# Kernel tuning notes

Hardware: AMD Instinct MI355X
Metric: run time of the kernel (lower is better)

## Reference

```python
import jax, jax.numpy as jnp
import numpy as np

N, S, D = 512, 64, 128   # num_nodes, seq_len, model_size
H, K = 4, 32             # num_heads, key_size
E = 4096                 # num_edges
WF = 4                   # widening_factor
EPS = 1e-5


def _alibi(num_heads, seq_len):
    slopes = 2.0 ** (-8.0 * (jnp.arange(1, num_heads + 1, dtype=jnp.float32) / num_heads))
    pos = jnp.arange(seq_len, dtype=jnp.float32)
    rel = pos[None, :] - pos[:, None]  # T - t, <= 0 in causal region
    return (slopes[:, None, None] * rel)[None]  # [1,H,S,S]


def layer_norm(x, scale, offset):
    mu = jnp.mean(x, axis=-1, keepdims=True)
    var = jnp.var(x, axis=-1, keepdims=True)
    return (x - mu) * jax.lax.rsqrt(var + EPS) * scale + offset


def segment_softmax(logits, seg, num_segments):
    maxs = jax.ops.segment_max(logits, seg, num_segments=num_segments)
    e = jnp.exp(logits - maxs[seg])
    denom = jax.ops.segment_sum(e, seg, num_segments=num_segments)
    return e / denom[seg]


def setup_inputs() -> dict:
    key = jax.random.key(0)
    ks = jax.random.split(key, 24)
    sd = 0.02
    inp = {
        'nodes': jax.random.normal(ks[0], (N, S, D), jnp.float32),
        'senders': jax.random.randint(ks[1], (E,), 0, N, jnp.int32),
        'receivers': jax.random.randint(ks[2], (E,), 0, N, jnp.int32),
        'alibi_mask': _alibi(H, S),
        'ln1_s': jnp.ones((D,)), 'ln1_b': jnp.zeros((D,)),
        'wq': jax.random.normal(ks[3], (D, H * K)) * sd, 'bq': jnp.zeros((H * K,)),
        'wk': jax.random.normal(ks[4], (D, H * K)) * sd, 'bk': jnp.zeros((H * K,)),
        'wv': jax.random.normal(ks[5], (D, H * K)) * sd, 'bv': jnp.zeros((H * K,)),
        'wo': jax.random.normal(ks[6], (H * K, D)) * sd, 'bo': jnp.zeros((D,)),
        'ln2_s': jnp.ones((D,)), 'ln2_b': jnp.zeros((D,)),
        'w1': jax.random.normal(ks[7], (D, WF * D)) * sd, 'b1': jnp.zeros((WF * D,)),
        'w2': jax.random.normal(ks[8], (WF * D, D)) * sd, 'b2': jnp.zeros((D,)),
        'ln3_s': jnp.ones((D,)), 'ln3_b': jnp.zeros((D,)),
        'w_sa': jax.random.normal(ks[9], (2 * D, D)) * sd, 'b_sa': jnp.zeros((D,)),
        'w_sq': jax.random.normal(ks[10], (D, H * D)) * sd, 'b_sq': jnp.zeros((H * D,)),
    }
    return inp


def reference(nodes, senders, receivers, alibi_mask,
              ln1_s, ln1_b, wq, bq, wk, bk, wv, bv, wo, bo,
              ln2_s, ln2_b, w1, b1, w2, b2, ln3_s, ln3_b,
              w_sa, b_sa, w_sq, b_sq):
    n, s, d = nodes.shape
    # --- node self-attention with ALiBi + causal mask ---
    xn = layer_norm(nodes, ln1_s, ln1_b)
    q = (xn @ wq + bq).reshape(n, s, H, K)
    k = (xn @ wk + bk).reshape(n, s, H, K)
    v = (xn @ wv + bv).reshape(n, s, H, K)
    logits = jnp.einsum('nthk,nThk->nhtT', q, k)
    logits = alibi_mask + logits / jnp.sqrt(jnp.float32(K))
    causal = jnp.tril(jnp.ones((1, 1, s, s), dtype=bool))
    logits = jnp.where(causal, logits, -1e30)
    w = jax.nn.softmax(logits, axis=-1)
    attn = jnp.einsum('nhtT,nThk->nthk', w, v).reshape(n, s, H * K)
    nodes = nodes + (attn @ wo + bo)  # dropout rate 0 (eval)
    # --- FFN block ---
    xn = layer_norm(nodes, ln2_s, ln2_b)
    dense = jax.nn.gelu(xn @ w1 + b1) @ w2 + b2
    nodes = layer_norm(nodes + dense, ln3_s, ln3_b)
    # --- graph message passing: gather / segment-softmax / segment-sum ---
    sent = nodes[senders]        # [E,S,D]
    recv = nodes[receivers]      # [E,S,D]
    sl = jnp.concatenate([sent, recv], axis=-1) @ w_sa + b_sa  # [E,S,D]
    aw = segment_softmax(sl, receivers, n)                     # [E,S,D]
    sq = (aw @ w_sq + b_sq).reshape(E, s, H, d)                # [E,S,H,D]
    messages = jnp.mean(sq * sent[:, :, None, :], axis=2)      # [E,S,D]
    out = jax.ops.segment_sum(messages, receivers, num_segments=n)
    return out
```

## Files before the change

kernel.cpp:

```cpp
#include <hip/hip_runtime.h>
#include <hip/hip_bf16.h>

typedef __hip_bfloat16 bf16;
typedef __attribute__((ext_vector_type(8))) __bf16 bf8v;
typedef __attribute__((ext_vector_type(4))) float  f4v;

#define NN 512
#define SSEQ 64
#define DDIM 128
#define HH 4
#define NROWS (NN*SSEQ)
#define EMAX 4096
#define ECH 64

__device__ __forceinline__ float b2f(bf16 x){ return __bfloat162float(x); }
__device__ __forceinline__ bf16 f2b(float x){ return __float2bfloat16(x); }
__device__ __forceinline__ float ldf(float x){ return x; }
__device__ __forceinline__ float ldf(bf16 x){ return b2f(x); }
__device__ __forceinline__ void stf(float* p, float v){ *p = v; }
__device__ __forceinline__ void stf(bf16* p, float v){ *p = f2b(v); }

__device__ __forceinline__ f4v mfma16(bf8v a, bf8v b, f4v c){
  return __builtin_amdgcn_mfma_f32_16x16x32_bf16(a, b, c, 0, 0, 0);
}
__device__ __forceinline__ bf8v ldfrag(const void* p){
  return __builtin_bit_cast(bf8v, *(const int4*)p);
}
__device__ __forceinline__ float gelu_f(float v){
  return 0.5f*v*(1.0f + tanhf(0.7978845608028654f*(v + 0.044715f*v*v*v)));
}

__global__ __launch_bounds__(512) void prep_all_k(
    const float* wq, const float* wk, const float* wv, const float* wo,
    const float* w1, const float* w2, const float* wsa,
    const float* w_sq, const float* b_sq,
    const float* bq, const float* bk, const float* bv,
    const int* __restrict__ receivers,
    bf16* wqkvT, bf16* woT, bf16* w1T, bf16* w2T, bf16* wsaTt,
    bf16* wbarT, float* bbar, float* qkv_bias,
    int* off, int* perm, int* chunk_cnt, int E){
  int b = blockIdx.x, t = threadIdx.x;
  if (b < 832){
    if (t >= 256) return;
    const float* W; bf16* Wt; int K, lN, rel, roff = 0;
    if      (b < 64) { W=wq;  Wt=wqkvT; K=128; lN=7; rel=b;     roff=0;   }
    else if (b <128) { W=wk;  Wt=wqkvT; K=128; lN=7; rel=b-64;  roff=128; }
    else if (b <192) { W=wv;  Wt=wqkvT; K=128; lN=7; rel=b-128; roff=256; }
    else if (b <256) { W=wo;  Wt=woT;   K=128; lN=7; rel=b-192; }
    else if (b <512) { W=w1;  Wt=w1T;   K=128; lN=9; rel=b-256; }
    else if (b <768) { W=w2;  Wt=w2T;   K=512; lN=7; rel=b-512; }
    else             { W=wsa; Wt=wsaTt; K=128; lN=7; rel=b-768; }
    int i = rel*256 + t;
    int k = i >> lN, n = i & ((1<<lN)-1);
    Wt[(size_t)(n+roff)*K + k] = f2b(W[i]);
  } else if (b < 896){
    if (t >= 256) return;
    int i = (b-832)*256 + t;
    int c = i>>7, d = i&127;
    float s = 0.f;
    #pragma unroll
    for (int h=0;h<HH;++h) s += w_sq[(size_t)c*(HH*DDIM) + h*DDIM + d];
    wbarT[d*DDIM + c] = f2b(0.25f*s);
  } else if (b < 898){
    if (t >= 256) return;
    int idx = (b-896)*256 + t;
    if (idx < 128){
      float s = 0.f;
      #pragma unroll
      for (int h=0;h<HH;++h) s += b_sq[h*DDIM + idx];
      bbar[idx] = 0.25f*s;
    } else if (idx < 512){
      int j = idx - 128;
      float v = (j<128) ? bq[j] : (j<256) ? bk[j-128] : bv[j-256];
      qkv_bias[j] = v;
    }
  } else if (b == 898){
    __shared__ int s_cnt[NN];
    s_cnt[t] = 0;
    __syncthreads();
    for (int e=t; e<E; e+=512) atomicAdd(&s_cnt[receivers[e]], 1);
    __syncthreads();
    int deg = s_cnt[t];
    int acc = 0, myrank = 0;
    for (int i=0;i<NN;++i){
      int di = s_cnt[i];
      acc    += (i<t) ? di : 0;
      myrank += ((di > deg) || (di == deg && i < t)) ? 1 : 0;
    }
    off[t] = acc;
    if (t==NN-1) off[NN] = acc + deg;
    perm[myrank] = t;
  } else {
    __shared__ int hc[NN];
    int c = b - 899;
    for (int i=t;i<NN;i+=512) hc[i]=0;
    __syncthreads();
    if (t < ECH){
      int e = c*ECH + t;
      if (e < E) atomicAdd(&hc[receivers[e]], 1);
    }
    __syncthreads();
    for (int i=t;i<NN;i+=512) chunk_cnt[(size_t)c*NN + i] = hc[i];
  }
}

__global__ __launch_bounds__(64) void slot_k(const int* __restrict__ senders,
    const int* __restrict__ receivers, const int* __restrict__ off,
    const int* __restrict__ chunk_cnt, int* __restrict__ slot_snd, int E){
  int t = threadIdx.x, c = blockIdx.x;
  int e = c*ECH + t;
  bool valid = (e < E);
  int r  = valid ? receivers[e] : -1;
  int sd = valid ? senders[e]   : 0;
  int base = 0;
  if (valid){
    base = off[r];
    for (int cp=0; cp<c; ++cp) base += chunk_cnt[(size_t)cp*NN + r];
  }
  int rank = 0;
  #pragma unroll
  for (int i=0;i<64;++i){
    int ri = __shfl(r, i);
    rank += (i < t && ri == r) ? 1 : 0;
  }
  if (valid) slot_snd[base + rank] = sd;
}

__global__ __launch_bounds__(256) void gemm_ln1qkv_k(const float* __restrict__ X,
    const float* __restrict__ lns, const float* __restrict__ lnb,
    const bf16* __restrict__ Wt, const float* __restrict__ bias,
    bf16* __restrict__ C){
  __shared__ bf16 sA[64][136];
  __shared__ bf16 sB[64][72];
  int t = threadIdx.x, bm = blockIdx.x;
  int w = t>>6, lane = t&63, ls = lane&15, lg = lane>>4;
  int wr = w>>1, wc = w&1;
  {
    int r = t>>2, q = t&3;
    float vals[32];
    const float* xr = X + (size_t)(bm*64 + r)*DDIM + q*32;
    #pragma unroll
    for (int p=0;p<8;++p){
      float4 v = *(const float4*)(xr + p*4);
      vals[p*4+0]=v.x; vals[p*4+1]=v.y; vals[p*4+2]=v.z; vals[p*4+3]=v.w;
    }
    float s=0.f, sq=0.f;
    #pragma unroll
    for (int j=0;j<32;++j){ s += vals[j]; sq += vals[j]*vals[j]; }
    s  += __shfl_xor(s, 1);  s  += __shfl_xor(s, 2);
    sq += __shfl_xor(sq, 1); sq += __shfl_xor(sq, 2);
    float mu   = s*(1.0f/DDIM);
    float var  = sq*(1.0f/DDIM) - mu*mu;
    float rstd = rsqrtf(var + 1e-5f);
    #pragma unroll
    for (int p=0;p<4;++p){
      bf16 pv[8];
      #pragma unroll
      for (int j=0;j<8;++j){
        int cidx = q*32 + p*8 + j;
        pv[j] = f2b((vals[p*8+j]-mu)*rstd*lns[cidx] + lnb[cidx]);
      }
      *(int4*)(&sA[r][q*32 + p*8]) = *(const int4*)pv;
    }
  }
  for (int bn=0; bn<6; ++bn){
    f4v acc[2][2] = {};
    for (int ks=0; ks<128; ks+=64){
      __syncthreads();
      #pragma unroll
      for (int p=0;p<2;++p){
        int r = p*32 + (t>>3), cc = (t&7)*8;
        *(int4*)(&sB[r][cc]) = *(const int4*)(Wt + (size_t)(bn*64+r)*128 + ks + cc);
      }
      __syncthreads();
      #pragma unroll
      for (int k0=0;k0<64;k0+=32){
        int kc = ks + k0 + 8*lg;
        bf8v a0 = ldfrag(&sA[wr*32      + ls][kc]);
        bf8v a1 = ldfrag(&sA[wr*32 + 16 + ls][kc]);
        bf8v b0 = ldfrag(&sB[wc*32      + ls][k0 + 8*lg]);
        bf8v b1 = ldfrag(&sB[wc*32 + 16 + ls][k0 + 8*lg]);
        acc[0][0] = mfma16(a0, b0, acc[0][0]);
        acc[0][1] = mfma16(a0, b1, acc[0][1]);
        acc[1][0] = mfma16(a1, b0, acc[1][0]);
        acc[1][1] = mfma16(a1, b1, acc[1][1]);
      }
    }
    #pragma unroll
    for (int j=0;j<2;++j){
      int gcol = bn*64 + wc*32 + j*16 + ls;
      float bs = bias[gcol];
      #pragma unroll
      for (int i=0;i<2;++i)
        #pragma unroll
        for (int r=0;r<4;++r){
          int grow = bm*64 + wr*32 + i*16 + 4*lg + r;
          C[(size_t)grow*384 + gcol] = f2b(acc[i][j][r] + bs);
        }
    }
  }
}

template<int KT, int ACT, typename TR, bool RES, bool BIAS>
__global__ __launch_bounds__(256) void gemm_m(const bf16* __restrict__ A,
    const bf16* __restrict__ Wt, const float* __restrict__ bias,
    const TR* __restrict__ R, bf16* __restrict__ C, int N){
  __shared__ bf16 sA[64][72];
  __shared__ bf16 sB[64][72];
  int t = threadIdx.x;
  int bm = blockIdx.x, bn = blockIdx.y;
  int w = t>>6, lane = t&63;
  int wr = w>>1, wc = w&1;
  f4v acc[2][2] = {};
  for (int ks=0; ks<KT; ks+=64){
    #pragma unroll
    for (int p=0;p<2;++p){
      int r = p*32 + (t>>3), cc = (t&7)*8;
      *(int4*)(&sA[r][cc]) = *(const int4*)(A  + (size_t)(bm*64+r)*KT + ks + cc);
      *(int4*)(&sB[r][cc]) = *(const int4*)(Wt + (size_t)(bn*64+r)*KT + ks + cc);
    }
    __syncthreads();
    #pragma unroll
    for (int k0=0;k0<64;k0+=32){
      int kc = k0 + 8*(lane>>4);
      bf8v a0 = ldfrag(&sA[wr*32      + (lane&15)][kc]);
      bf8v a1 = ldfrag(&sA[wr*32 + 16 + (lane&15)][kc]);
      bf8v b0 = ldfrag(&sB[wc*32      + (lane&15)][kc]);
      bf8v b1 = ldfrag(&sB[wc*32 + 16 + (lane&15)][kc]);
      acc[0][0] = mfma16(a0, b0, acc[0][0]);
      acc[0][1] = mfma16(a0, b1, acc[0][1]);
      acc[1][0] = mfma16(a1, b0, acc[1][0]);
      acc[1][1] = mfma16(a1, b1, acc[1][1]);
    }
    __syncthreads();
  }
  #pragma unroll
  for (int j=0;j<2;++j){
    int gcol = bn*64 + wc*32 + j*16 + (lane&15);
    float bs = BIAS ? bias[gcol] : 0.f;
    #pragma unroll
    for (int i=0;i<2;++i){
      #pragma unroll
      for (int r=0;r<4;++r){
        int grow = bm*64 + wr*32 + i*16 + 4*(lane>>4) + r;
        float v = acc[i][j][r] + bs;
        if (ACT==1) v = gelu_f(v);
        if (ACT==2) v = __expf(v);
        if (RES) v += ldf(R[(size_t)grow*N + gcol]);
        C[(size_t)grow*N + gcol] = f2b(v);
      }
    }
  }
}

__global__ __launch_bounds__(256) void gemm_wo_ln2_k(const bf16* __restrict__ A,
    const bf16* __restrict__ Wt, const float* __restrict__ bias,
    const float* __restrict__ Rres, const float* __restrict__ lns,
    const float* __restrict__ lnb, bf16* __restrict__ n2out,
    bf16* __restrict__ xnout){
  __shared__ bf16 sA[64][72];
  __shared__ bf16 sB[128][72];
  __shared__ float s_st[2][2][32][2];
  int t = threadIdx.x, bm = blockIdx.x;
  int w = t>>6, lane = t&63, ls = lane&15, lg = lane>>4;
  int wr = w>>1, wc = w&1;
  f4v acc[2][4] = {};
  for (int ks=0; ks<128; ks+=64){
    #pragma unroll
    for (int p=0;p<2;++p){
      int r = p*32 + (t>>3), cc = (t&7)*8;
      *(int4*)(&sA[r][cc]) = *(const int4*)(A + (size_t)(bm*64+r)*128 + ks + cc);
    }
    #pragma unroll
    for (int p=0;p<4;++p){
      int r = p*32 + (t>>3), cc = (t&7)*8;
      *(int4*)(&sB[r][cc]) = *(const int4*)(Wt + (size_t)r*128 + ks + cc);
    }
    __syncthreads();
    #pragma unroll
    for (int k0=0;k0<64;k0+=32){
      int kc = k0 + 8*lg;
      bf8v a0 = ldfrag(&sA[wr*32      + ls][kc]);
      bf8v a1 = ldfrag(&sA[wr*32 + 16 + ls][kc]);
      #pragma unroll
      for (int j=0;j<4;++j){
        bf8v bj = ldfrag(&sB[wc*64 + j*16 + ls][kc]);
        acc[0][j] = mfma16(a0, bj, acc[0][j]);
        acc[1][j] = mfma16(a1, bj, acc[1][j]);
      }
    }
    __syncthreads();
  }
  float x[2][4][4];
  float psum[2][4], psq[2][4];
  #pragma unroll
  for (int i=0;i<2;++i)
    #pragma unroll
    for (int r=0;r<4;++r){ psum[i][r]=0.f; psq[i][r]=0.f; }
  #pragma unroll
  for (int i=0;i<2;++i){
    #pragma unroll
    for (int j=0;j<4;++j){
      int col = wc*64 + j*16 + ls;
      float bs = bias[col];
      #pragma unroll
      for (int r=0;r<4;++r){
        int row = bm*64 + wr*32 + i*16 + 4*lg + r;
        float v = acc[i][j][r] + bs + Rres[(size_t)row*128 + col];
        x[i][j][r] = v;
        psum[i][r] += v;
        psq[i][r]  += v*v;
        n2out[(size_t)row*128 + col] = f2b(v);
      }
    }
  }
  #pragma unroll
  for (int i=0;i<2;++i)
    #pragma unroll
    for (int r=0;r<4;++r){
      float s_=psum[i][r], q_=psq[i][r];
      s_ += __shfl_xor(s_,1); s_ += __shfl_xor(s_,2);
      s_ += __shfl_xor(s_,4); s_ += __shfl_xor(s_,8);
      q_ += __shfl_xor(q_,1); q_ += __shfl_xor(q_,2);
      q_ += __shfl_xor(q_,4); q_ += __shfl_xor(q_,8);
      if (ls == 0){
        int rl = i*16 + 4*lg + r;
        s_st[wr][wc][rl][0] = s_;
        s_st[wr][wc][rl][1] = q_;
      }
    }
  __syncthreads();
  #pragma unroll
  for (int i=0;i<2;++i){
    #pragma unroll
    for (int r=0;r<4;++r){
      int rl = i*16 + 4*lg + r;
      float s_ = s_st[wr][0][rl][0] + s_st[wr][1][rl][0];
      float q_ = s_st[wr][0][rl][1] + s_st[wr][1][rl][1];
      float mu = s_*(1.0f/DDIM);
      float var = q_*(1.0f/DDIM) - mu*mu;
      float rstd = rsqrtf(var + 1e-5f);
      int row = bm*64 + wr*32 + rl;
      #pragma unroll
      for (int j=0;j<4;++j){
        int col = wc*64 + j*16 + ls;
        xnout[(size_t)row*128 + col] = f2b((x[i][j][r]-mu)*rstd*lns[col] + lnb[col]);
      }
    }
  }
}

__global__ __launch_bounds__(256) void gemm_w2_tail_k(const bf16* __restrict__ A,
    const bf16* __restrict__ Wt, const float* __restrict__ bias,
    const bf16* __restrict__ Rres, const float* __restrict__ lns,
    const float* __restrict__ lnb, const bf16* __restrict__ wsaT,
    bf16* __restrict__ r2out, bf16* __restrict__ yexpout){
  __shared__ bf16 sA[64][72];
  __shared__ bf16 sB[128][72];
  __shared__ bf16 sY[64][136];
  __shared__ float s_st[2][2][32][2];
  int t = threadIdx.x, bm = blockIdx.x;
  int w = t>>6, lane = t&63, ls = lane&15, lg = lane>>4;
  int wr = w>>1, wc = w&1;
  f4v acc[2][4] = {};
  for (int ks=0; ks<512; ks+=64){
    #pragma unroll
    for (int p=0;p<2;++p){
      int r = p*32 + (t>>3), cc = (t&7)*8;
      *(int4*)(&sA[r][cc]) = *(const int4*)(A + (size_t)(bm*64+r)*512 + ks + cc);
    }
    #pragma unroll
    for (int p=0;p<4;++p){
      int r = p*32 + (t>>3), cc = (t&7)*8;
      *(int4*)(&sB[r][cc]) = *(const int4*)(Wt + (size_t)r*512 + ks + cc);
    }
    __syncthreads();
    #pragma unroll
    for (int k0=0;k0<64;k0+=32){
      int kc = k0 + 8*lg;
      bf8v a0 = ldfrag(&sA[wr*32      + ls][kc]);
      bf8v a1 = ldfrag(&sA[wr*32 + 16 + ls][kc]);
      #pragma unroll
      for (int j=0;j<4;++j){
        bf8v bj = ldfrag(&sB[wc*64 + j*16 + ls][kc]);
        acc[0][j] = mfma16(a0, bj, acc[0][j]);
        acc[1][j] = mfma16(a1, bj, acc[1][j]);
      }
    }
    __syncthreads();
  }
  float x[2][4][4];
  float psum[2][4], psq[2][4];
  #pragma unroll
  for (int i=0;i<2;++i)
    #pragma unroll
    for (int r=0;r<4;++r){ psum[i][r]=0.f; psq[i][r]=0.f; }
  #pragma unroll
  for (int i=0;i<2;++i){
    #pragma unroll
    for (int j=0;j<4;++j){
      int col = wc*64 + j*16 + ls;
      float bs = bias[col];
      #pragma unroll
      for (int r=0;r<4;++r){
        int row = bm*64 + wr*32 + i*16 + 4*lg + r;
        float v = acc[i][j][r] + bs + b2f(Rres[(size_t)row*128 + col]);
        x[i][j][r] = v;
        psum[i][r] += v;
        psq[i][r]  += v*v;
      }
    }
  }
  #pragma unroll
  for (int i=0;i<2;++i)
    #pragma unroll
    for (int r=0;r<4;++r){
      float s_=psum[i][r], q_=psq[i][r];
      s_ += __shfl_xor(s_,1); s_ += __shfl_xor(s_,2);
      s_ += __shfl_xor(s_,4); s_ += __shfl_xor(s_,8);
      q_ += __shfl_xor(q_,1); q_ += __shfl_xor(q_,2);
      q_ += __shfl_xor(q_,4); q_ += __shfl_xor(q_,8);
      if (ls == 0){
        int rl = i*16 + 4*lg + r;
        s_st[wr][wc][rl][0] = s_;
        s_st[wr][wc][rl][1] = q_;
      }
    }
  __syncthreads();
  #pragma unroll
  for (int i=0;i<2;++i){
    #pragma unroll
    for (int r=0;r<4;++r){
      int rl = i*16 + 4*lg + r;
      float s_ = s_st[wr][0][rl][0] + s_st[wr][1][rl][0];
      float q_ = s_st[wr][0][rl][1] + s_st[wr][1][rl][1];
      float mu = s_*(1.0f/DDIM);
      float var = q_*(1.0f/DDIM) - mu*mu;
      float rstd = rsqrtf(var + 1e-5f);
      int row = bm*64 + wr*32 + rl;
      #pragma unroll
      for (int j=0;j<4;++j){
        int col = wc*64 + j*16 + ls;
        bf16 yb = f2b((x[i][j][r]-mu)*rstd*lns[col] + lnb[col]);
        r2out[(size_t)row*128 + col] = yb;
        sY[wr*32 + rl][col] = yb;
      }
    }
  }
  __syncthreads();
  f4v acc2[2][4] = {};
  for (int ks2=0; ks2<128; ks2+=64){
    #pragma unroll
    for (int p=0;p<4;++p){
      int r = p*32 + (t>>3), cc = (t&7)*8;
      *(int4*)(&sB[r][cc]) = *(const int4*)(wsaT + (size_t)r*128 + ks2 + cc);
    }
    __syncthreads();
    #pragma unroll
    for (int k0=0;k0<64;k0+=32){
      int kc = k0 + 8*lg;
      bf8v a0 = ldfrag(&sY[wr*32      + ls][ks2 + kc]);
      bf8v a1 = ldfrag(&sY[wr*32 + 16 + ls][ks2 + kc]);
      #pragma unroll
      for (int j=0;j<4;++j){
        bf8v bj = ldfrag(&sB[wc*64 + j*16 + ls][kc]);
        acc2[0][j] = mfma16(a0, bj, acc2[0][j]);
        acc2[1][j] = mfma16(a1, bj, acc2[1][j]);
      }
    }
    __syncthreads();
  }
  #pragma unroll
  for (int i=0;i<2;++i){
    #pragma unroll
    for (int j=0;j<4;++j){
      int col = wc*64 + j*16 + ls;
      #pragma unroll
      for (int r=0;r<4;++r){
        int row = bm*64 + wr*32 + i*16 + 4*lg + r;
        yexpout[(size_t)row*128 + col] = f2b(__expf(acc2[i][j][r]));
      }
    }
  }
}

__global__ __launch_bounds__(256) void attn_m(const bf16* __restrict__ qkvb,
    bf16* __restrict__ ob){
  __shared__ bf16 sVT[128][72];
  __shared__ bf16 sP[4][64][72];
  int t = threadIdx.x, n = blockIdx.x;
  int w = t>>6, lane = t&63, ls = lane&15, lg = lane>>4;
  const bf16* qbase = qkvb + (size_t)n*SSEQ*(3*DDIM);
  bf8v qf[4], kf[4];
  #pragma unroll
  for (int mi=0;mi<4;++mi)
    qf[mi] = ldfrag(qbase + (size_t)(16*mi + ls)*(3*DDIM) + 32*w + 8*lg);
  #pragma unroll
  for (int ni=0;ni<4;++ni)
    kf[ni] = ldfrag(qbase + (size_t)(16*ni + ls)*(3*DDIM) + DDIM + 32*w + 8*lg);
  for (int id = t; id < 1024; id += 256){
    int T = id>>4, c = id&15;
    int4 v = *(const int4*)(qbase + (size_t)T*(3*DDIM) + 2*DDIM + c*8);
    const bf16* pv = (const bf16*)&v;
    #pragma unroll
    for (int j=0;j<8;++j){
      int d = c*8 + j;
      sVT[d][T ^ (((d>>3)&7)<<3)] = pv[j];
    }
  }
  f4v accS[4][4];
  #pragma unroll
  for (int mi=0;mi<4;++mi)
    #pragma unroll
    for (int ni=0;ni<4;++ni){
      f4v z = {};
      accS[mi][ni] = mfma16(qf[mi], kf[ni], z);
    }
  __syncthreads();
  const float scale = 0.17677669529663687f;
  const float slope = 1.0f / (float)(4 << (2*w));
  float den[4][4];
  #pragma unroll
  for (int mi=0;mi<4;++mi)
    #pragma unroll
    for (int r=0;r<4;++r) den[mi][r] = 0.f;
  #pragma unroll
  for (int mi=0;mi<4;++mi){
    #pragma unroll
    for (int ni=0;ni<4;++ni){
      #pragma unroll
      for (int r=0;r<4;++r){
        int rel = (16*ni + ls) - (16*mi + 4*lg + r);
        float p = (rel <= 0) ? __expf(accS[mi][ni][r]*scale + slope*(float)rel) : 0.f;
        accS[mi][ni][r] = p;
        den[mi][r] += p;
      }
    }
  }
  #pragma unroll
  for (int mi=0;mi<4;++mi)
    #pragma unroll
    for (int r=0;r<4;++r){
      float d_ = den[mi][r];
      d_ += __shfl_xor(d_, 1);  d_ += __shfl_xor(d_, 2);
      d_ += __shfl_xor(d_, 4);  d_ += __shfl_xor(d_, 8);
      den[mi][r] = 1.0f / d_;
    }
  #pragma unroll
  for (int mi=0;mi<4;++mi)
    #pragma unroll
    for (int ni=0;ni<4;++ni)
      #pragma unroll
      for (int r=0;r<4;++r)
        sP[w][16*mi + 4*lg + r][16*ni + ls] = f2b(accS[mi][ni][r]*den[mi][r]);
  f4v oacc[4][2] = {};
  #pragma unroll
  for (int ks=0;ks<2;++ks){
    bf8v vf[2];
    #pragma unroll
    for (int ni2=0;ni2<2;++ni2){
      int d = 32*w + 16*ni2 + ls;
      vf[ni2] = ldfrag(&sVT[d][(32*ks + 8*lg) ^ (((d>>3)&7)<<3)]);
    }
    #pragma unroll
    for (int mi=0;mi<4;++mi){
      bf8v pa = ldfrag(&sP[w][16*mi + ls][32*ks + 8*lg]);
      #pragma unroll
      for (int ni2=0;ni2<2;++ni2)
        oacc[mi][ni2] = mfma16(pa, vf[ni2], oacc[mi][ni2]);
    }
  }
  #pragma unroll
  for (int mi=0;mi<4;++mi)
    #pragma unroll
    for (int ni2=0;ni2<2;++ni2)
      #pragma unroll
      for (int r=0;r<4;++r)
        ob[(size_t)(n*SSEQ + 16*mi + 4*lg + r)*DDIM + 32*w + 16*ni2 + ls]
          = f2b(oacc[mi][ni2][r]);
}

__global__ __launch_bounds__(256) void msg4_k(const bf16* __restrict__ yexp,
    const bf16* __restrict__ nodes3, const int* __restrict__ off,
    const int* __restrict__ slot_snd, const int* __restrict__ perm,
    const bf16* __restrict__ wbarT, const float* __restrict__ bbar,
    float* __restrict__ out){
  __shared__ bf16 sP[2][16][136];
  __shared__ bf16 s_sent[4][3][16][36];
  int t = threadIdx.x, sc = blockIdx.y;
  int n = perm[blockIdx.x];
  int w = t>>6, lane = t&63, ls = lane&15, lg = lane>>4;
  int off0 = off[n], deg = off[n+1]-off0;
  int dbase = w*32;
  if (deg == 0){
    #pragma unroll
    for (int ct=0;ct<2;++ct)
      #pragma unroll
      for (int r=0;r<4;++r)
        out[((size_t)n*SSEQ + sc*16 + 4*lg + r)*DDIM + dbase + ct*16 + ls] = 0.f;
    return;
  }
  bf8v B[2][4];
  #pragma unroll
  for (int ct=0;ct<2;++ct)
    #pragma unroll
    for (int kb=0;kb<4;++kb)
      B[ct][kb] = ldfrag(wbarT + (size_t)(dbase + ct*16 + ls)*DDIM + kb*32 + lg*8);
  float bb[2];
  #pragma unroll
  for (int ct=0;ct<2;++ct) bb[ct] = bbar[dbase + ct*16 + ls];
  int rp = t>>4, cp = (t&15)*8;
  size_t prow = ((size_t)(sc*16 + rp))*DDIM + cp;
  float den8[8];
  #pragma unroll
  for (int j=0;j<8;++j) den8[j] = 0.f;
  {
    int k = 0;
    for (; k+2<=deg; k+=2){
      int s0 = slot_snd[off0+k], s1 = slot_snd[off0+k+1];
      int4 v0 = *(const int4*)(yexp + (size_t)s0*SSEQ*DDIM + prow);
      int4 v1 = *(const int4*)(yexp + (size_t)s1*SSEQ*DDIM + prow);
      const bf16* a = (const bf16*)&v0;
      const bf16* b = (const bf16*)&v1;
      #pragma unroll
      for (int j=0;j<8;++j) den8[j] += b2f(a[j]) + b2f(b[j]);
    }
    if (k < deg){
      int s0 = slot_snd[off0+k];
      int4 v = *(const int4*)(yexp + (size_t)s0*SSEQ*DDIM + prow);
      const bf16* a = (const bf16*)&v;
      #pragma unroll
      for (int j=0;j<8;++j) den8[j] += b2f(a[j]);
    }
  }
  #pragma unroll
  for (int j=0;j<8;++j) den8[j] = 1.0f/den8[j];
  int rs = lane>>2, cs = (lane&3)*8;
  int4 yv1;
  {
    int snd = slot_snd[off0];
    int4 v = *(const int4*)(yexp + (size_t)snd*SSEQ*DDIM + prow);
    const bf16* a = (const bf16*)&v;
    bf16 pv[8];
    #pragma unroll
    for (int j=0;j<8;++j) pv[j] = f2b(b2f(a[j]) * den8[j]);
    *(int4*)&sP[0][rp][cp] = *(const int4*)pv;
    *(int4*)&s_sent[w][0][rs][cs] =
      *(const int4*)(nodes3 + ((size_t)snd*SSEQ + sc*16 + rs)*DDIM + dbase + cs);
  }
  if (deg > 1){
    int snd = slot_snd[off0+1];
    yv1 = *(const int4*)(yexp + (size_t)snd*SSEQ*DDIM + prow);
    *(int4*)&s_sent[w][1][rs][cs] =
      *(const int4*)(nodes3 + ((size_t)snd*SSEQ + sc*16 + rs)*DDIM + dbase + cs);
  }
  __syncthreads();
  f4v oacc[2] = {};
  int4 yvN;
  for (int k=0;k<deg;++k){
    int buf = k&1;
    if (k+2 < deg){
      int snd2 = slot_snd[off0+k+2];
      yvN = *(const int4*)(yexp + (size_t)snd2*SSEQ*DDIM + prow);
      *(int4*)&s_sent[w][(k+2)%3][rs][cs] =
        *(const int4*)(nodes3 + ((size_t)snd2*SSEQ + sc*16 + rs)*DDIM + dbase + cs);
    }
    if (k+1 < deg){
      const bf16* a = (const bf16*)&yv1;
      bf16 pv[8];
      #pragma unroll
      for (int j=0;j<8;++j) pv[j] = f2b(b2f(a[j]) * den8[j]);
      *(int4*)&sP[buf^1][rp][cp] = *(const int4*)pv;
    }
    bf8v a4[4];
    #pragma unroll
    for (int kb=0;kb<4;++kb) a4[kb] = ldfrag(&sP[buf][ls][kb*32 + lg*8]);
    f4v g[2] = {};
    #pragma unroll
    for (int kb=0;kb<4;++kb)
      #pragma unroll
      for (int ct=0;ct<2;++ct)
        g[ct] = mfma16(a4[kb], B[ct][kb], g[ct]);
    #pragma unroll
    for (int ct=0;ct<2;++ct)
      #pragma unroll
      for (int r=0;r<4;++r){
        float sent = b2f(s_sent[w][k%3][4*lg + r][ct*16 + ls]);
        oacc[ct][r] += (g[ct][r] + bb[ct]) * sent;
      }
    __syncthreads();
    yv1 = yvN;
  }
  #pragma unroll
  for (int ct=0;ct<2;++ct)
    #pragma unroll
    for (int r=0;r<4;++r)
      out[((size_t)n*SSEQ + sc*16 + 4*lg + r)*DDIM + dbase + ct*16 + ls] = oacc[ct][r];
}

extern "C" void kernel_launch(void* const* d_in, const int* in_sizes, int n_in,
                              void* d_out, int out_size, void* d_ws, size_t ws_size,
                              hipStream_t stream){
  const float* nodes = (const float*)d_in[0];
  const int*  senders   = (const int*)d_in[1];
  const int*  receivers = (const int*)d_in[2];
  const float* ln1_s=(const float*)d_in[4];  const float* ln1_b=(const float*)d_in[5];
  const float* wq=(const float*)d_in[6];     const float* bq=(const float*)d_in[7];
  const float* wk=(const float*)d_in[8];     const float* bk=(const float*)d_in[9];
  const float* wv=(const float*)d_in[10];    const float* bv_=(const float*)d_in[11];
  const float* wo=(const float*)d_in[12];    const float* bo=(const float*)d_in[13];
  const float* ln2_s=(const float*)d_in[14]; const float* ln2_b=(const float*)d_in[15];
  const float* w1=(const float*)d_in[16];    const float* b1=(const float*)d_in[17];
  const float* w2=(const float*)d_in[18];    const float* b2=(const float*)d_in[19];
  const float* ln3_s=(const float*)d_in[20]; const float* ln3_b=(const float*)d_in[21];
  const float* w_sa=(const float*)d_in[22];
  const float* w_sq=(const float*)d_in[24];  const float* b_sq=(const float*)d_in[25];
  int E = in_sizes[1];
  int nch = (E + ECH - 1)/ECH;

  const size_t MB = 1024*1024;
  char* ws = (char*)d_ws;
  bf16* attnout = (bf16*)(ws);
  bf16* qkvb    = (bf16*)(ws +  8*MB);
  bf16* n2      = (bf16*)(ws + 32*MB);
  bf16* xn2     = (bf16*)(ws + 48*MB);
  bf16* hb      = (bf16*)(ws);
  bf16* r2     = (bf16*)(ws + 64*MB);
  bf16* yexp   = (bf16*)(ws + 72*MB);
  char* tail = ws + 88*MB;
  bf16*  wbarT   = (bf16*)tail;                       tail += DDIM*DDIM*2;
  float* bbar    = (float*)tail;                      tail += DDIM*4 + 512;
  float* qkv_bias= (float*)tail;                      tail += 3*DDIM*4;
  int*   off     = (int*)tail;                        tail += (NN+8)*4;
  int*   slot_snd= (int*)tail;                        tail += EMAX*4;
  int*   perm    = (int*)tail;                        tail += NN*4;
  int*   ccnt    = (int*)tail;                        tail += 64*NN*4;
  bf16*  wqkvT   = (bf16*)tail;                       tail += 384*128*2;
  bf16*  woT     = (bf16*)tail;                       tail += 128*128*2;
  bf16*  w1T     = (bf16*)tail;                       tail += 128*512*2;
  bf16*  w2T     = (bf16*)tail;                       tail += 512*128*2;
  bf16*  wsaTt   = (bf16*)tail;                       tail += 128*128*2;

  prep_all_k<<<899+nch,512,0,stream>>>(wq,wk,wv,wo,w1,w2,w_sa,w_sq,b_sq,bq,bk,bv_,
                                       receivers,
                                       wqkvT,woT,w1T,w2T,wsaTt,wbarT,bbar,qkv_bias,
                                       off, perm, ccnt, E);
  slot_k<<<nch,64,0,stream>>>(senders, receivers, off, ccnt, slot_snd, E);

  gemm_ln1qkv_k<<<NROWS/64,256,0,stream>>>(nodes, ln1_s, ln1_b, wqkvT, qkv_bias, qkvb);
  attn_m<<<NN,256,0,stream>>>(qkvb, attnout);
  gemm_wo_ln2_k<<<NROWS/64,256,0,stream>>>(attnout, woT, bo, nodes, ln2_s, ln2_b, n2, xn2);
  gemm_m<128,1,bf16,false,true><<<dim3(NROWS/64,8),256,0,stream>>>(xn2, w1T, b1, (const bf16*)nullptr, hb, 512);
  gemm_w2_tail_k<<<NROWS/64,256,0,stream>>>(hb, w2T, b2, n2, ln3_s, ln3_b, wsaTt, r2, yexp);

  msg4_k<<<dim3(NN,4),256,0,stream>>>(yexp, r2, off, slot_snd, perm, wbarT, bbar, (float*)d_out);
}
```

Baseline: 145.1 us.

## Fuse causal attention with output projection and LayerNorm into one kernel

Result: faster. 141.3 us (-2.6%).

```diff
diff --git a/kernel.cpp b/kernel.cpp
--- a/kernel.cpp
+++ b/kernel.cpp
@@ -253,43 +253,129 @@
   }
 }
 
-__global__ __launch_bounds__(256) void gemm_wo_ln2_k(const bf16* __restrict__ A,
-    const bf16* __restrict__ Wt, const float* __restrict__ bias,
+__global__ __launch_bounds__(256) void attn_wo_k(const bf16* __restrict__ qkvb,
+    const bf16* __restrict__ woT, const float* __restrict__ bias,
     const float* __restrict__ Rres, const float* __restrict__ lns,
     const float* __restrict__ lnb, bf16* __restrict__ n2out,
     bf16* __restrict__ xnout){
-  __shared__ bf16 sA[64][72];
+  __shared__ bf16 sVT[128][72];
+  __shared__ bf16 sP[4][64][72];
   __shared__ bf16 sB[128][72];
   __shared__ float s_st[2][2][32][2];
-  int t = threadIdx.x, bm = blockIdx.x;
+  bf16 (*sAtt)[136] = (bf16(*)[136])(&sP[0][0][0]);
+  int t = threadIdx.x, n = blockIdx.x;
   int w = t>>6, lane = t&63, ls = lane&15, lg = lane>>4;
+  const bf16* qbase = qkvb + (size_t)n*SSEQ*(3*DDIM);
+  bf8v qf[4], kf[4];
+  #pragma unroll
+  for (int mi=0;mi<4;++mi)
+    qf[mi] = ldfrag(qbase + (size_t)(16*mi + ls)*(3*DDIM) + 32*w + 8*lg);
+  #pragma unroll
+  for (int ni=0;ni<4;++ni)
+    kf[ni] = ldfrag(qbase + (size_t)(16*ni + ls)*(3*DDIM) + DDIM + 32*w + 8*lg);
+  for (int id = t; id < 1024; id += 256){
+    int T = id>>4, c = id&15;
+    int4 v = *(const int4*)(qbase + (size_t)T*(3*DDIM) + 2*DDIM + c*8);
+    const bf16* pv = (const bf16*)&v;
+    #pragma unroll
+    for (int j=0;j<8;++j){
+      int d = c*8 + j;
+      sVT[d][T ^ (((d>>3)&7)<<3)] = pv[j];
+    }
+  }
+  f4v accS[4][4];
+  #pragma unroll
+  for (int mi=0;mi<4;++mi)
+    #pragma unroll
+    for (int ni=0;ni<4;++ni){
+      f4v z = {};
+      accS[mi][ni] = mfma16(qf[mi], kf[ni], z);
+    }
+  __syncthreads();
+  const float scale = 0.17677669529663687f;
+  const float slope = 1.0f / (float)(4 << (2*w));
+  float den[4][4];
+  #pragma unroll
+  for (int mi=0;mi<4;++mi)
+    #pragma unroll
+    for (int r=0;r<4;++r) den[mi][r] = 0.f;
+  #pragma unroll
+  for (int mi=0;mi<4;++mi){
+    #pragma unroll
+    for (int ni=0;ni<4;++ni){
+      #pragma unroll
+      for (int r=0;r<4;++r){
+        int rel = (16*ni + ls) - (16*mi + 4*lg + r);
+        float p = (rel <= 0) ? __expf(accS[mi][ni][r]*scale + slope*(float)rel) : 0.f;
+        accS[mi][ni][r] = p;
+        den[mi][r] += p;
+      }
+    }
+  }
+  #pragma unroll
+  for (int mi=0;mi<4;++mi)
+    #pragma unroll
+    for (int r=0;r<4;++r){
+      float d_ = den[mi][r];
+      d_ += __shfl_xor(d_, 1);  d_ += __shfl_xor(d_, 2);
+      d_ += __shfl_xor(d_, 4);  d_ += __shfl_xor(d_, 8);
+      den[mi][r] = 1.0f / d_;
+    }
+  #pragma unroll
+  for (int mi=0;mi<4;++mi)
+    #pragma unroll
+    for (int ni=0;ni<4;++ni)
+      #pragma unroll
+      for (int r=0;r<4;++r)
+        sP[w][16*mi + 4*lg + r][16*ni + ls] = f2b(accS[mi][ni][r]*den[mi][r]);
+  f4v oacc[4][2] = {};
+  #pragma unroll
+  for (int ks=0;ks<2;++ks){
+    bf8v vf[2];
+    #pragma unroll
+    for (int ni2=0;ni2<2;++ni2){
+      int d = 32*w + 16*ni2 + ls;
+      vf[ni2] = ldfrag(&sVT[d][(32*ks + 8*lg) ^ (((d>>3)&7)<<3)]);
+    }
+    #pragma unroll
+    for (int mi=0;mi<4;++mi){
+      bf8v pa = ldfrag(&sP[w][16*mi + ls][32*ks + 8*lg]);
+      #pragma unroll
+      for (int ni2=0;ni2<2;++ni2)
+        oacc[mi][ni2] = mfma16(pa, vf[ni2], oacc[mi][ni2]);
+    }
+  }
+  __syncthreads();
+  #pragma unroll
+  for (int mi=0;mi<4;++mi)
+    #pragma unroll
+    for (int ni2=0;ni2<2;++ni2)
+      #pragma unroll
+      for (int r=0;r<4;++r)
+        sAtt[16*mi + 4*lg + r][32*w + 16*ni2 + ls] = f2b(oacc[mi][ni2][r]);
+  __syncthreads();
   int wr = w>>1, wc = w&1;
-  f4v acc[2][4] = {};
+  f4v acc2[2][4] = {};
   for (int ks=0; ks<128; ks+=64){
-    #pragma unroll
-    for (int p=0;p<2;++p){
-      int r = p*32 + (t>>3), cc = (t&7)*8;
-      *(int4*)(&sA[r][cc]) = *(const int4*)(A + (size_t)(bm*64+r)*128 + ks + cc);
-    }
+    if (ks) __syncthreads();
     #pragma unroll
     for (int p=0;p<4;++p){
       int r = p*32 + (t>>3), cc = (t&7)*8;
-      *(int4*)(&sB[r][cc]) = *(const int4*)(Wt + (size_t)r*128 + ks + cc);
+      *(int4*)(&sB[r][cc]) = *(const int4*)(woT + (size_t)r*128 + ks + cc);
     }
     __syncthreads();
     #pragma unroll
     for (int k0=0;k0<64;k0+=32){
-      int kc = k0 + 8*lg;
-      bf8v a0 = ldfrag(&sA[wr*32      + ls][kc]);
-      bf8v a1 = ldfrag(&sA[wr*32 + 16 + ls][kc]);
+      int kc = ks + k0 + 8*lg;
+      bf8v a0 = ldfrag(&sAtt[wr*32      + ls][kc]);
+      bf8v a1 = ldfrag(&sAtt[wr*32 + 16 + ls][kc]);
       #pragma unroll
       for (int j=0;j<4;++j){
-        bf8v bj = ldfrag(&sB[wc*64 + j*16 + ls][kc]);
-        acc[0][j] = mfma16(a0, bj, acc[0][j]);
-        acc[1][j] = mfma16(a1, bj, acc[1][j]);
-      }
-    }
-    __syncthreads();
+        bf8v bj = ldfrag(&sB[wc*64 + j*16 + ls][k0 + 8*lg]);
+        acc2[0][j] = mfma16(a0, bj, acc2[0][j]);
+        acc2[1][j] = mfma16(a1, bj, acc2[1][j]);
+      }
+    }
   }
   float x[2][4][4];
   float psum[2][4], psq[2][4];
@@ -305,8 +391,8 @@
       float bs = bias[col];
       #pragma unroll
       for (int r=0;r<4;++r){
-        int row = bm*64 + wr*32 + i*16 + 4*lg + r;
-        float v = acc[i][j][r] + bs + Rres[(size_t)row*128 + col];
+        int row = n*64 + wr*32 + i*16 + 4*lg + r;
+        float v = acc2[i][j][r] + bs + Rres[(size_t)row*128 + col];
         x[i][j][r] = v;
         psum[i][r] += v;
         psq[i][r]  += v*v;
@@ -340,7 +426,7 @@
       float mu = s_*(1.0f/DDIM);
       float var = q_*(1.0f/DDIM) - mu*mu;
       float rstd = rsqrtf(var + 1e-5f);
-      int row = bm*64 + wr*32 + rl;
+      int row = n*64 + wr*32 + rl;
       #pragma unroll
       for (int j=0;j<4;++j){
         int col = wc*64 + j*16 + ls;
@@ -482,102 +568,6 @@
       }
     }
   }
-}
-
-__global__ __launch_bounds__(256) void attn_m(const bf16* __restrict__ qkvb,
-    bf16* __restrict__ ob){
-  __shared__ bf16 sVT[128][72];
-  __shared__ bf16 sP[4][64][72];
-  int t = threadIdx.x, n = blockIdx.x;
-  int w = t>>6, lane = t&63, ls = lane&15, lg = lane>>4;
-  const bf16* qbase = qkvb + (size_t)n*SSEQ*(3*DDIM);
-  bf8v qf[4], kf[4];
-  #pragma unroll
-  for (int mi=0;mi<4;++mi)
-    qf[mi] = ldfrag(qbase + (size_t)(16*mi + ls)*(3*DDIM) + 32*w + 8*lg);
-  #pragma unroll
-  for (int ni=0;ni<4;++ni)
-    kf[ni] = ldfrag(qbase + (size_t)(16*ni + ls)*(3*DDIM) + DDIM + 32*w + 8*lg);
-  for (int id = t; id < 1024; id += 256){
-    int T = id>>4, c = id&15;
-    int4 v = *(const int4*)(qbase + (size_t)T*(3*DDIM) + 2*DDIM + c*8);
-    const bf16* pv = (const bf16*)&v;
-    #pragma unroll
-    for (int j=0;j<8;++j){
-      int d = c*8 + j;
-      sVT[d][T ^ (((d>>3)&7)<<3)] = pv[j];
-    }
-  }
-  f4v accS[4][4];
-  #pragma unroll
-  for (int mi=0;mi<4;++mi)
-    #pragma unroll
-    for (int ni=0;ni<4;++ni){
-      f4v z = {};
-      accS[mi][ni] = mfma16(qf[mi], kf[ni], z);
-    }
-  __syncthreads();
-  const float scale = 0.17677669529663687f;
-  const float slope = 1.0f / (float)(4 << (2*w));
-  float den[4][4];
-  #pragma unroll
-  for (int mi=0;mi<4;++mi)
-    #pragma unroll
-    for (int r=0;r<4;++r) den[mi][r] = 0.f;
-  #pragma unroll
-  for (int mi=0;mi<4;++mi){
-    #pragma unroll
-    for (int ni=0;ni<4;++ni){
-      #pragma unroll
-      for (int r=0;r<4;++r){
-        int rel = (16*ni + ls) - (16*mi + 4*lg + r);
-        float p = (rel <= 0) ? __expf(accS[mi][ni][r]*scale + slope*(float)rel) : 0.f;
-        accS[mi][ni][r] = p;
-        den[mi][r] += p;
-      }
-    }
-  }
-  #pragma unroll
-  for (int mi=0;mi<4;++mi)
-    #pragma unroll
-    for (int r=0;r<4;++r){
-      float d_ = den[mi][r];
-      d_ += __shfl_xor(d_, 1);  d_ += __shfl_xor(d_, 2);
-      d_ += __shfl_xor(d_, 4);  d_ += __shfl_xor(d_, 8);
-      den[mi][r] = 1.0f / d_;
-    }
-  #pragma unroll
-  for (int mi=0;mi<4;++mi)
-    #pragma unroll
-    for (int ni=0;ni<4;++ni)
-      #pragma unroll
-      for (int r=0;r<4;++r)
-        sP[w][16*mi + 4*lg + r][16*ni + ls] = f2b(accS[mi][ni][r]*den[mi][r]);
-  f4v oacc[4][2] = {};
-  #pragma unroll
-  for (int ks=0;ks<2;++ks){
-    bf8v vf[2];
-    #pragma unroll
-    for (int ni2=0;ni2<2;++ni2){
-      int d = 32*w + 16*ni2 + ls;
-      vf[ni2] = ldfrag(&sVT[d][(32*ks + 8*lg) ^ (((d>>3)&7)<<3)]);
-    }
-    #pragma unroll
-    for (int mi=0;mi<4;++mi){
-      bf8v pa = ldfrag(&sP[w][16*mi + ls][32*ks + 8*lg]);
-      #pragma unroll
-      for (int ni2=0;ni2<2;++ni2)
-        oacc[mi][ni2] = mfma16(pa, vf[ni2], oacc[mi][ni2]);
-    }
-  }
-  #pragma unroll
-  for (int mi=0;mi<4;++mi)
-    #pragma unroll
-    for (int ni2=0;ni2<2;++ni2)
-      #pragma unroll
-      for (int r=0;r<4;++r)
-        ob[(size_t)(n*SSEQ + 16*mi + 4*lg + r)*DDIM + 32*w + 16*ni2 + ls]
-          = f2b(oacc[mi][ni2][r]);
 }
 
 __global__ __launch_bounds__(256) void msg4_k(const bf16* __restrict__ yexp,
@@ -720,7 +710,6 @@
 
   const size_t MB = 1024*1024;
   char* ws = (char*)d_ws;
-  bf16* attnout = (bf16*)(ws);
   bf16* qkvb    = (bf16*)(ws +  8*MB);
   bf16* n2      = (bf16*)(ws + 32*MB);
   bf16* xn2     = (bf16*)(ws + 48*MB);
@@ -748,8 +737,7 @@
   slot_k<<<nch,64,0,stream>>>(senders, receivers, off, ccnt, slot_snd, E);
 
   gemm_ln1qkv_k<<<NROWS/64,256,0,stream>>>(nodes, ln1_s, ln1_b, wqkvT, qkv_bias, qkvb);
-  attn_m<<<NN,256,0,stream>>>(qkvb, attnout);
-  gemm_wo_ln2_k<<<NROWS/64,256,0,stream>>>(attnout, woT, bo, nodes, ln2_s, ln2_b, n2, xn2);
+  attn_wo_k<<<NN,256,0,stream>>>(qkvb, woT, bo, nodes, ln2_s, ln2_b, n2, xn2);
   gemm_m<128,1,bf16,false,true><<<dim3(NROWS/64,8),256,0,stream>>>(xn2, w1T, b1, (const bf16*)nullptr, hb, 512);
   gemm_w2_tail_k<<<NROWS/64,256,0,stream>>>(hb, w2T, b2, n2, ln3_s, ln3_b, wsaTt, r2, yexp);
 
```
